# Kernel optimization log

Measured on AMD Instinct MI355X. Metric: run time of the kernel, lower is better.

The kernel has to match this reference:

```python
import math
import jax, jax.numpy as jnp
import numpy as np

N_HEAD = 16

def setup_inputs() -> dict:
    key = jax.random.key(0)
    ks = jax.random.split(key, 6)
    B, T, C = 8, 2048, 1024
    x = jax.random.normal(ks[0], (B, T, C), dtype=jnp.float32)
    # Linear weights stored as (in, out); scaled ~ standard init
    W_attn = jax.random.normal(ks[1], (C, 3 * C), dtype=jnp.float32) * (1.0 / math.sqrt(C))
    b_attn = jnp.zeros((3 * C,), dtype=jnp.float32)
    W_proj = jax.random.normal(ks[2], (C, C), dtype=jnp.float32) * (1.0 / math.sqrt(C))
    b_proj = jnp.zeros((C,), dtype=jnp.float32)
    # E/F: torch.randn in the original; scale by 0.02 so softmax is non-degenerate
    E = jax.random.normal(ks[3], (N_HEAD, 128, T), dtype=jnp.float32) * 0.02
    F = jax.random.normal(ks[4], (N_HEAD, 128, T), dtype=jnp.float32) * 0.02
    return {"x": x, "W_attn": W_attn, "b_attn": b_attn,
            "W_proj": W_proj, "b_proj": b_proj, "E": E, "F": F}

def reference(x, W_attn, b_attn, W_proj, b_proj, E, F):
    B, T, C = x.shape
    H = N_HEAD
    D = C // H
    scale = 1.0 / math.sqrt(D)
    qkv = x @ W_attn + b_attn                       # [B,T,3C]
    q, k, v = jnp.split(qkv, 3, axis=-1)
    # [B,T,C] -> [B,H,T,D]
    q = q.reshape(B, T, H, D).transpose(0, 2, 1, 3)
    k = k.reshape(B, T, H, D).transpose(0, 2, 1, 3)
    v = v.reshape(B, T, H, D).transpose(0, 2, 1, 3)
    Et = E[:, :, :T]                                # [H,k,T]
    Ft = F[:, :, :T]
    k_proj = jnp.einsum('hkt,bhtd->bhkd', Et, k)    # [B,H,k,D]
    v_proj = jnp.einsum('hkt,bhtd->bhkd', Ft, v)
    att = jnp.einsum('bhtd,bhkd->bhtk', q, k_proj) * scale
    att = jax.nn.softmax(att, axis=-1)              # dropout p=0 -> identity
    y = jnp.einsum('bhtk,bhkd->bhtd', att, v_proj)
    y = y.transpose(0, 2, 1, 3).reshape(B, T, C)
    return y @ W_proj + b_proj
```

## Files before the change

kernel.cpp:

```cpp
#include <hip/hip_runtime.h>
#include <math.h>


constexpr int B_ = 8, T_ = 2048, C_ = 1024, H_ = 16, D_ = 64, KP = 128;
constexpr int M_ = B_ * T_;
constexpr int C3 = 3 * C_;
constexpr int K_ = C_;
constexpr int TCH = 4;

typedef __attribute__((ext_vector_type(8))) short bf16x8;
typedef __attribute__((ext_vector_type(4))) float f32x4;

__device__ __forceinline__ unsigned short f2bf(float f) {
  unsigned u = __builtin_bit_cast(unsigned, f);
  u += 0x7FFFu + ((u >> 16) & 1u);
  return (unsigned short)(u >> 16);
}
__device__ __forceinline__ float bf2f(unsigned short h) {
  unsigned u = ((unsigned)h) << 16;
  return __builtin_bit_cast(float, u);
}

#define GLOAD_LDS16(gptr, lptr)                                                \
  __builtin_amdgcn_global_load_lds(                                            \
      (const __attribute__((address_space(1))) void*)(gptr),                   \
      (__attribute__((address_space(3))) void*)(lptr), 16, 0, 0)

__global__ __launch_bounds__(256) void cast_bf16(
    const float* __restrict__ in, unsigned short* __restrict__ hi, int n4)
{
  int i = blockIdx.x * 256 + threadIdx.x;
  if (i >= n4) return;
  const float4 v = reinterpret_cast<const float4*>(in)[i];
  ushort4 h;
  h.x = f2bf(v.x); h.y = f2bf(v.y); h.z = f2bf(v.z); h.w = f2bf(v.w);
  reinterpret_cast<ushort4*>(hi)[i] = h;
}

__global__ __launch_bounds__(256) void cast_tr(
    const float* __restrict__ W, unsigned short* __restrict__ Tb,
    int rows, int cols)
{
  __shared__ float tile[32][33];
  const int c0 = blockIdx.x * 32, r0 = blockIdx.y * 32;
  const int tx = threadIdx.x & 31, ty = threadIdx.x >> 5;
  #pragma unroll
  for (int i = 0; i < 4; ++i)
    tile[ty + i * 8][tx] = W[(size_t)(r0 + ty + i * 8) * cols + c0 + tx];
  __syncthreads();
  #pragma unroll
  for (int i = 0; i < 4; ++i) {
    const int cr = ty + i * 8;
    Tb[(size_t)(c0 + cr) * rows + r0 + tx] = f2bf(tile[tx][cr]);
  }
}

template <bool BFOUT>
__global__ __launch_bounds__(256) void gemm_mfma1(
    const unsigned short* __restrict__ A, const unsigned short* __restrict__ BT,
    const float* __restrict__ bias, float* __restrict__ Cf,
    unsigned short* __restrict__ Cb, int ldc)
{
  __shared__ unsigned short lds[2 * 4096];
  unsigned short* sA = lds;
  unsigned short* sB = lds + 4096;

  const int tid  = threadIdx.x;
  const int lane = tid & 63;
  const int wid  = tid >> 6;
  const int m0 = blockIdx.y * 128;
  const int n0 = blockIdx.x * 128;

  const int srow  = lane >> 2;
  const int skseg = (lane & 3) << 3;
  const int col  = lane & 15;
  const int quad = lane >> 4;
  const int Rm = (wid >> 1) << 6;
  const int Rn = (wid & 1) << 6;

  f32x4 acc[4][4];
  #pragma unroll
  for (int i = 0; i < 4; ++i)
    #pragma unroll
    for (int j = 0; j < 4; ++j)
      acc[i][j] = (f32x4){0.f, 0.f, 0.f, 0.f};

  for (int k0 = 0; k0 < K_; k0 += 32) {
    #pragma unroll
    for (int r = 0; r < 2; ++r) {
      const int chunk = (r << 2) + wid;
      const int row = (chunk << 4) + srow;
      const int ldso = chunk << 9;
      GLOAD_LDS16(A + (size_t)(m0 + row) * K_ + k0 + skseg, sA + ldso);
      GLOAD_LDS16(BT + (size_t)(n0 + row) * K_ + k0 + skseg, sB + ldso);
    }
    __syncthreads();

    bf16x8 a[4], b[4];
    #pragma unroll
    for (int t = 0; t < 4; ++t) {
      a[t] = *reinterpret_cast<const bf16x8*>(
          sA + ((Rm + (t << 4) + col) << 5) + (quad << 3));
      b[t] = *reinterpret_cast<const bf16x8*>(
          sB + ((Rn + (t << 4) + col) << 5) + (quad << 3));
    }
    #pragma unroll
    for (int i = 0; i < 4; ++i)
      #pragma unroll
      for (int j = 0; j < 4; ++j)
        acc[i][j] = __builtin_amdgcn_mfma_f32_16x16x32_bf16(a[i], b[j], acc[i][j], 0, 0, 0);
    __syncthreads();
  }

  #pragma unroll
  for (int i = 0; i < 4; ++i) {
    const int rbase = m0 + Rm + (i << 4) + (quad << 2);
    #pragma unroll
    for (int j = 0; j < 4; ++j) {
      const int c = n0 + Rn + (j << 4) + col;
      const float bv = bias[c];
      #pragma unroll
      for (int rg = 0; rg < 4; ++rg) {
        const float v = acc[i][j][rg] + bv;
        const size_t o = (size_t)(rbase + rg) * ldc + c;
        if constexpr (BFOUT) Cb[o] = f2bf(v);
        else Cf[o] = v;
      }
    }
  }
}

__global__ __launch_bounds__(256) void proj_mfma(
    const unsigned short* __restrict__ Eh, const unsigned short* __restrict__ kb,
    int ldk, float* __restrict__ part)
{
  __shared__ unsigned short sE[KP * 72];
  __shared__ unsigned short sK[D_ * 72];

  const int bh = blockIdx.x;
  const int tc = blockIdx.y;
  const int b = bh >> 4, h = bh & 15;
  const int tid = threadIdx.x;
  const int lane = tid & 63;
  const int w = tid >> 6;
  const int col = lane & 15;
  const int quad = lane >> 4;
  const int tq = tid >> 4;
  const int dq = tid & 15;

  f32x4 acc[2][4];
  #pragma unroll
  for (int i = 0; i < 2; ++i)
    #pragma unroll
    for (int j = 0; j < 4; ++j) acc[i][j] = (f32x4){0.f, 0.f, 0.f, 0.f};

  for (int s = 0; s < 8; ++s) {
    const int t0 = tc * 512 + s * 64;
    #pragma unroll
    for (int l = 0; l < 4; ++l) {
      const int idx = l * 256 + tid;
      const int kk = idx >> 3, seg = idx & 7;
      *reinterpret_cast<uint4*>(sE + kk * 72 + seg * 8) =
          *reinterpret_cast<const uint4*>(
              Eh + (size_t)(h * KP + kk) * T_ + t0 + seg * 8);
    }
    {
      const size_t gbase = (size_t)(b * T_ + t0 + tq * 4) * ldk + h * D_ + dq * 4;
      ushort4 r[4];
      #pragma unroll
      for (int rr = 0; rr < 4; ++rr)
        r[rr] = *reinterpret_cast<const ushort4*>(kb + gbase + (size_t)rr * ldk);
      #pragma unroll
      for (int c = 0; c < 4; ++c) {
        ushort4 t;
        t.x = (&r[0].x)[c]; t.y = (&r[1].x)[c];
        t.z = (&r[2].x)[c]; t.w = (&r[3].x)[c];
        *reinterpret_cast<ushort4*>(sK + (dq * 4 + c) * 72 + tq * 4) = t;
      }
    }
    __syncthreads();

    bf16x8 av[2][2];
    #pragma unroll
    for (int i = 0; i < 2; ++i)
      #pragma unroll
      for (int ks = 0; ks < 2; ++ks)
        av[i][ks] = *reinterpret_cast<const bf16x8*>(
            sE + ((w * 2 + i) * 16 + col) * 72 + ks * 32 + quad * 8);
    #pragma unroll
    for (int j = 0; j < 4; ++j)
      #pragma unroll
      for (int ks = 0; ks < 2; ++ks) {
        const bf16x8 bv = *reinterpret_cast<const bf16x8*>(
            sK + (j * 16 + col) * 72 + ks * 32 + quad * 8);
        #pragma unroll
        for (int i = 0; i < 2; ++i)
          acc[i][j] = __builtin_amdgcn_mfma_f32_16x16x32_bf16(av[i][ks], bv, acc[i][j], 0, 0, 0);
      }
    __syncthreads();
  }

  float* op = part + ((size_t)bh * TCH + tc) * (KP * D_);
  #pragma unroll
  for (int i = 0; i < 2; ++i) {
    const int kkb = w * 32 + i * 16 + quad * 4;
    #pragma unroll
    for (int j = 0; j < 4; ++j) {
      const int d = j * 16 + col;
      #pragma unroll
      for (int rg = 0; rg < 4; ++rg)
        op[(kkb + rg) * D_ + d] = acc[i][j][rg];
    }
  }
}

__global__ __launch_bounds__(256) void reduce_k(
    const float* __restrict__ part, unsigned short* __restrict__ kprojh)
{
  const int idx = blockIdx.x * 256 + threadIdx.x;
  const int bh = idx >> 13;
  const int i = idx & 8191;
  float s = 0.f;
  #pragma unroll
  for (int c = 0; c < TCH; ++c)
    s += part[((size_t)bh * TCH + c) * 8192 + i];
  kprojh[idx] = f2bf(s);
}

__global__ __launch_bounds__(256) void reduce_v(
    const float* __restrict__ part, unsigned short* __restrict__ vpTh)
{
  __shared__ float sums[KP * 66];
  const int bh = blockIdx.x;
  const int tid = threadIdx.x;
  #pragma unroll
  for (int j = 0; j < 32; ++j) {
    const int i = j * 256 + tid;
    float s = 0.f;
    #pragma unroll
    for (int c = 0; c < TCH; ++c)
      s += part[((size_t)bh * TCH + c) * 8192 + i];
    sums[(i >> 6) * 66 + (i & 63)] = s;
  }
  __syncthreads();
  #pragma unroll
  for (int j = 0; j < 32; ++j) {
    const int i = j * 256 + tid;
    vpTh[(size_t)bh * 8192 + i] = f2bf(sums[(i & 127) * 66 + (i >> 7)]);
  }
}

__global__ __launch_bounds__(256) void attn_mfma(
    const unsigned short* __restrict__ qkv, const unsigned short* __restrict__ kprojh,
    const unsigned short* __restrict__ vpTh, unsigned short* __restrict__ yh)
{
  __shared__ __attribute__((aligned(16))) char lds[35072];
  unsigned short* Qh = (unsigned short*)(lds);
  unsigned short* Kp = (unsigned short*)(lds + 9216);
  unsigned short* Vh = (unsigned short*)(lds);
  unsigned short* Ps = (unsigned short*)(lds + 17408);
  float* atts = (float*)(lds + 34816);

  const int tid  = threadIdx.x;
  const int lane = tid & 63;
  const int w    = tid >> 6;
  const int col  = lane & 15;
  const int quad = lane >> 4;
  const int bh = blockIdx.x >> 5;
  const int tch = blockIdx.x & 31;
  const int b = bh >> 4, h = bh & 15;
  const int t0 = tch * 64;

  {
    const unsigned short* qg = qkv + (size_t)(b * T_ + t0) * C3 + h * D_;
    #pragma unroll
    for (int l = 0; l < 4; ++l) {
      const int idx = l * 256 + tid;
      const int t = idx >> 4, dc = (idx & 15) << 2;
      *reinterpret_cast<ushort4*>(Qh + t * 72 + dc) =
          *reinterpret_cast<const ushort4*>(qg + (size_t)t * C3 + dc);
    }
    const unsigned short* kg = kprojh + (size_t)bh * 8192;
    #pragma unroll
    for (int l = 0; l < 8; ++l) {
      const int idx = l * 256 + tid;
      const int kk = idx >> 4, dc = (idx & 15) << 2;
      *reinterpret_cast<ushort4*>(Kp + kk * 72 + dc) =
          *reinterpret_cast<const ushort4*>(kg + kk * 64 + dc);
    }
  }
  __syncthreads();

  f32x4 s[8];
  #pragma unroll
  for (int i = 0; i < 8; ++i) s[i] = (f32x4){0.f, 0.f, 0.f, 0.f};
  bf16x8 bq[2];
  #pragma unroll
  for (int ks = 0; ks < 2; ++ks)
    bq[ks] = *reinterpret_cast<const bf16x8*>(
        Qh + (w * 16 + col) * 72 + ks * 32 + quad * 8);
  #pragma unroll
  for (int i = 0; i < 8; ++i)
    #pragma unroll
    for (int ks = 0; ks < 2; ++ks) {
      const bf16x8 a = *reinterpret_cast<const bf16x8*>(
          Kp + (i * 16 + col) * 72 + ks * 32 + quad * 8);
      s[i] = __builtin_amdgcn_mfma_f32_16x16x32_bf16(a, bq[ks], s[i], 0, 0, 0);
    }

  float mx = -3.0e38f;
  #pragma unroll
  for (int i = 0; i < 8; ++i)
    #pragma unroll
    for (int rg = 0; rg < 4; ++rg) {
      s[i][rg] *= 0.125f;
      mx = fmaxf(mx, s[i][rg]);
    }
  mx = fmaxf(mx, __shfl_xor(mx, 16));
  mx = fmaxf(mx, __shfl_xor(mx, 32));
  float sum = 0.f;
  #pragma unroll
  for (int i = 0; i < 8; ++i)
    #pragma unroll
    for (int rg = 0; rg < 4; ++rg) {
      const float e = __expf(s[i][rg] - mx);
      s[i][rg] = e;
      sum += e;
    }
  sum += __shfl_xor(sum, 16);
  sum += __shfl_xor(sum, 32);
  const float inv = 1.f / sum;
  __syncthreads();

  {
    const unsigned short* vg = vpTh + (size_t)bh * 8192;
    #pragma unroll
    for (int l = 0; l < 8; ++l) {
      const int idx = l * 256 + tid;
      const int d = idx >> 5, kc = (idx & 31) << 2;
      *reinterpret_cast<ushort4*>(Vh + d * 136 + kc) =
          *reinterpret_cast<const ushort4*>(vg + d * 128 + kc);
    }
  }
  #pragma unroll
  for (int i = 0; i < 8; ++i) {
    ushort4 hp;
    hp.x = f2bf(s[i][0]); hp.y = f2bf(s[i][1]);
    hp.z = f2bf(s[i][2]); hp.w = f2bf(s[i][3]);
    *reinterpret_cast<ushort4*>(Ps + (w * 16 + col) * 136 + i * 16 + quad * 4) = hp;
  }
  if (quad == 0) atts[w * 16 + col] = inv;
  __syncthreads();

  f32x4 y[4];
  #pragma unroll
  for (int j = 0; j < 4; ++j) y[j] = (f32x4){0.f, 0.f, 0.f, 0.f};
  bf16x8 ap[4];
  #pragma unroll
  for (int ks = 0; ks < 4; ++ks)
    ap[ks] = *reinterpret_cast<const bf16x8*>(
        Ps + (w * 16 + col) * 136 + ks * 32 + quad * 8);
  #pragma unroll
  for (int j = 0; j < 4; ++j)
    #pragma unroll
    for (int ks = 0; ks < 4; ++ks) {
      const bf16x8 bv = *reinterpret_cast<const bf16x8*>(
          Vh + (j * 16 + col) * 136 + ks * 32 + quad * 8);
      y[j] = __builtin_amdgcn_mfma_f32_16x16x32_bf16(ap[ks], bv, y[j], 0, 0, 0);
    }

  const f32x4 inv4 = *reinterpret_cast<const f32x4*>(atts + w * 16 + quad * 4);
  #pragma unroll
  for (int j = 0; j < 4; ++j)
    #pragma unroll
    for (int rg = 0; rg < 4; ++rg) {
      const int t = t0 + w * 16 + quad * 4 + rg;
      const int d = j * 16 + col;
      yh[(size_t)(b * T_ + t) * C_ + h * D_ + d] = f2bf(y[j][rg] * inv4[rg]);
    }
}

extern "C" void kernel_launch(void* const* d_in, const int* in_sizes, int n_in,
                              void* d_out, int out_size, void* d_ws, size_t ws_size,
                              hipStream_t stream) {
  (void)in_sizes; (void)n_in; (void)out_size; (void)ws_size;
  const float* x      = (const float*)d_in[0];
  const float* W_attn = (const float*)d_in[1];
  const float* b_attn = (const float*)d_in[2];
  const float* W_proj = (const float*)d_in[3];
  const float* b_proj = (const float*)d_in[4];
  const float* E      = (const float*)d_in[5];
  const float* F      = (const float*)d_in[6];
  float* out = (float*)d_out;

  unsigned short* xh   = (unsigned short*)d_ws;
  unsigned short* qkvh = xh + (size_t)M_ * C_;
  unsigned short* WaT  = qkvh + (size_t)M_ * C3;
  unsigned short* WpT  = WaT + (size_t)C3 * C_;
  unsigned short* Eh   = WpT + (size_t)C_ * C_;
  unsigned short* Fh   = Eh + (size_t)H_ * KP * T_;
  float* part = (float*)(Fh + (size_t)H_ * KP * T_);
  unsigned short* kprojh = (unsigned short*)(part + (size_t)B_ * H_ * TCH * KP * D_);
  unsigned short* vpTh   = kprojh + (size_t)B_ * H_ * KP * D_;
  unsigned short* yh = xh;

  cast_bf16<<<(M_ * C_ / 4 + 255) / 256, 256, 0, stream>>>(x, xh, M_ * C_ / 4);
  cast_bf16<<<(H_ * KP * T_ / 4 + 255) / 256, 256, 0, stream>>>(E, Eh, H_ * KP * T_ / 4);
  cast_bf16<<<(H_ * KP * T_ / 4 + 255) / 256, 256, 0, stream>>>(F, Fh, H_ * KP * T_ / 4);
  cast_tr<<<dim3(C3 / 32, C_ / 32), 256, 0, stream>>>(W_attn, WaT, C_, C3);
  cast_tr<<<dim3(C_ / 32, C_ / 32), 256, 0, stream>>>(W_proj, WpT, C_, C_);

  gemm_mfma1<true><<<dim3(C3 / 128, M_ / 128), 256, 0, stream>>>(
      xh, WaT, b_attn, nullptr, qkvh, C3);

  proj_mfma<<<dim3(B_ * H_, TCH), 256, 0, stream>>>(Eh, qkvh + C_, C3, part);
  reduce_k<<<(B_ * H_ * KP * D_) / 256, 256, 0, stream>>>(part, kprojh);

  proj_mfma<<<dim3(B_ * H_, TCH), 256, 0, stream>>>(Fh, qkvh + 2 * C_, C3, part);
  reduce_v<<<B_ * H_, 256, 0, stream>>>(part, vpTh);

  attn_mfma<<<B_ * H_ * (T_ / 64), 256, 0, stream>>>(qkvh, kprojh, vpTh, yh);

  gemm_mfma1<false><<<dim3(C_ / 128, M_ / 128), 256, 0, stream>>>(
      yh, WpT, b_proj, out, nullptr, C_);
}
```

Baseline: 416.1 us.

## Replace GEMM with 256x256 tile, 8-wave, double-buffered swizzled LDS pipeline

Swaps the 128x128 single-stage MFMA GEMM for a 256x256 tile kernel that uses 512 threads, a 64-wide K step and two 64KB LDS buffers. Global-to-LDS loads for later K tiles are interleaved with MFMA quadrants under explicit waitcnt and barrier control, and MFMA sections run at raised priority. The LDS layout is XOR-swizzled to avoid bank conflicts, and block IDs are remapped for L2 locality. The aim is more data reuse per byte loaded and overlap of load latency with compute in both large GEMMs. In exchange it relies on 128KB of LDS per block and fragile hand-written wait counts that could race or stall.

```diff
diff --git a/kernel.cpp b/kernel.cpp
--- a/kernel.cpp
+++ b/kernel.cpp
@@ -6,6 +6,7 @@
 constexpr int M_ = B_ * T_;
 constexpr int C3 = 3 * C_;
 constexpr int K_ = C_;
+constexpr int NT = K_ / 64;
 constexpr int TCH = 4;
 
 typedef __attribute__((ext_vector_type(8))) short bf16x8;
@@ -56,73 +57,172 @@
 }
 
 template <bool BFOUT>
-__global__ __launch_bounds__(256) void gemm_mfma1(
+__global__ __launch_bounds__(512, 2) void gemm256(
     const unsigned short* __restrict__ A, const unsigned short* __restrict__ BT,
     const float* __restrict__ bias, float* __restrict__ Cf,
     unsigned short* __restrict__ Cb, int ldc)
 {
-  __shared__ unsigned short lds[2 * 4096];
-  unsigned short* sA = lds;
-  unsigned short* sB = lds + 4096;
+  __shared__ __attribute__((aligned(16))) char lds[131072];
 
   const int tid  = threadIdx.x;
   const int lane = tid & 63;
-  const int wid  = tid >> 6;
-  const int m0 = blockIdx.y * 128;
-  const int n0 = blockIdx.x * 128;
-
-  const int srow  = lane >> 2;
-  const int skseg = (lane & 3) << 3;
+  const int w    = tid >> 6;
+  const int wr   = w >> 2;
+  const int wc   = w & 3;
   const int col  = lane & 15;
   const int quad = lane >> 4;
-  const int Rm = (wid >> 1) << 6;
-  const int Rn = (wid & 1) << 6;
-
-  f32x4 acc[4][4];
-  #pragma unroll
-  for (int i = 0; i < 4; ++i)
-    #pragma unroll
-    for (int j = 0; j < 4; ++j)
-      acc[i][j] = (f32x4){0.f, 0.f, 0.f, 0.f};
-
-  for (int k0 = 0; k0 < K_; k0 += 32) {
-    #pragma unroll
-    for (int r = 0; r < 2; ++r) {
-      const int chunk = (r << 2) + wid;
-      const int row = (chunk << 4) + srow;
-      const int ldso = chunk << 9;
-      GLOAD_LDS16(A + (size_t)(m0 + row) * K_ + k0 + skseg, sA + ldso);
-      GLOAD_LDS16(BT + (size_t)(n0 + row) * K_ + k0 + skseg, sB + ldso);
-    }
-    __syncthreads();
-
-    bf16x8 a[4], b[4];
-    #pragma unroll
-    for (int t = 0; t < 4; ++t) {
-      a[t] = *reinterpret_cast<const bf16x8*>(
-          sA + ((Rm + (t << 4) + col) << 5) + (quad << 3));
-      b[t] = *reinterpret_cast<const bf16x8*>(
-          sB + ((Rn + (t << 4) + col) << 5) + (quad << 3));
-    }
-    #pragma unroll
-    for (int i = 0; i < 4; ++i)
-      #pragma unroll
-      for (int j = 0; j < 4; ++j)
-        acc[i][j] = __builtin_amdgcn_mfma_f32_16x16x32_bf16(a[i], b[j], acc[i][j], 0, 0, 0);
-    __syncthreads();
-  }
-
-  #pragma unroll
-  for (int i = 0; i < 4; ++i) {
-    const int rbase = m0 + Rm + (i << 4) + (quad << 2);
-    #pragma unroll
-    for (int j = 0; j < 4; ++j) {
-      const int c = n0 + Rn + (j << 4) + col;
-      const float bv = bias[c];
+
+  const int ntx = ldc >> 8;
+  int wg = blockIdx.x;
+  wg = (wg & 7) * (gridDim.x >> 3) + (wg >> 3);
+  const int bx = wg % ntx, by = wg / ntx;
+  const int m0 = by << 8, n0 = bx << 8;
+
+  int mOff[2], nOff[2], csh[2];
+  #pragma unroll
+  for (int l = 0; l < 2; ++l) {
+    const int rl = w * 16 + l * 8 + (lane >> 3);
+    mOff[l] = (rl >> 6) * 128 + (rl & 63);
+    nOff[l] = (rl >> 5) * 64 + (rl & 31);
+    csh[l]  = ((lane & 7) * 8) ^ (((lane >> 5) & 1) << 4) ^ (l << 3);
+  }
+
+#define STAGE_A(H, KT0, BUFSEL)                                                \
+  { const int kb_ = (KT0) * 64;                                                \
+    _Pragma("unroll")                                                          \
+    for (int l = 0; l < 2; ++l)                                                \
+      GLOAD_LDS16(A + (size_t)(m0 + mOff[l] + (H) * 64) * K_ + kb_ + csh[l],   \
+                  lds + (BUFSEL) * 65536 + (H) * 16384 + w * 2048 + l * 1024); }
+
+#define STAGE_B(H, KT0, BUFSEL)                                                \
+  { const int kb_ = (KT0) * 64;                                                \
+    _Pragma("unroll")                                                          \
+    for (int l = 0; l < 2; ++l)                                                \
+      GLOAD_LDS16(BT + (size_t)(n0 + nOff[l] + (H) * 32) * K_ + kb_ + csh[l],  \
+                  lds + (BUFSEL) * 65536 + 32768 + (H) * 16384 + w * 2048 +    \
+                      l * 1024); }
+
+  const int qsw = (quad * 16) ^ ((col & 4) << 3) ^ ((col & 8) << 1);
+  const int aB0 = (wr * 64 + col) * 128;
+  const int aB1 = (128 + wr * 64 + col) * 128;
+  const int bB0 = 32768 + (wc * 32 + col) * 128;
+  const int bB1 = 32768 + (128 + wc * 32 + col) * 128;
+
+  f32x4 acc[8][4];
+  #pragma unroll
+  for (int a = 0; a < 8; ++a)
+    #pragma unroll
+    for (int c = 0; c < 4; ++c)
+      acc[a][c] = (f32x4){0.f, 0.f, 0.f, 0.f};
+
+  bf16x8 av[4][2], b0v[2][2], b1v[2][2];
+
+#define MFMA_Q(QM, QN, BV)                                                     \
+  __builtin_amdgcn_s_setprio(1);                                               \
+  _Pragma("unroll")                                                            \
+  for (int j = 0; j < 2; ++j)                                                  \
+    _Pragma("unroll")                                                          \
+    for (int ks = 0; ks < 2; ++ks)                                             \
+      _Pragma("unroll")                                                        \
+      for (int i = 0; i < 4; ++i)                                              \
+        acc[(QM) * 4 + i][(QN) * 2 + j] =                                      \
+            __builtin_amdgcn_mfma_f32_16x16x32_bf16(                           \
+                av[i][ks], BV[j][ks], acc[(QM) * 4 + i][(QN) * 2 + j], 0, 0, 0);\
+  __builtin_amdgcn_s_setprio(0);
+
+  STAGE_A(0, 0, 0);
+  STAGE_B(0, 0, 0);
+  STAGE_B(1, 0, 0);
+  STAGE_A(1, 0, 0);
+  asm volatile("s_waitcnt vmcnt(4)" ::: "memory");
+  STAGE_A(0, 1, 1);
+  STAGE_B(0, 1, 1);
+  STAGE_B(1, 1, 1);
+  asm volatile("s_waitcnt vmcnt(6)" ::: "memory");
+  __builtin_amdgcn_s_barrier();
+
+#define TILE(KT, CUR)                                                          \
+  {                                                                            \
+    const char* cb = lds + (CUR) * 65536;                                      \
+                       \
+    _Pragma("unroll")                                                          \
+    for (int i = 0; i < 4; ++i)                                                \
+      _Pragma("unroll")                                                        \
+      for (int ks = 0; ks < 2; ++ks)                                           \
+        av[i][ks] = *reinterpret_cast<const bf16x8*>(                          \
+            cb + aB0 + i * 2048 + ks * 64 + qsw);                              \
+    _Pragma("unroll")                                                          \
+    for (int j = 0; j < 2; ++j)                                                \
+      _Pragma("unroll")                                                        \
+      for (int ks = 0; ks < 2; ++ks)                                           \
+        b0v[j][ks] = *reinterpret_cast<const bf16x8*>(                         \
+            cb + bB0 + j * 2048 + ks * 64 + qsw);                              \
+    if ((KT) + 1 < NT) { STAGE_A(1, (KT) + 1, (CUR) ^ 1); }                    \
+    asm volatile("s_waitcnt lgkmcnt(8)" ::: "memory");                         \
+    __builtin_amdgcn_s_barrier();                                              \
+    asm volatile("s_waitcnt lgkmcnt(0)" ::: "memory");                         \
+    __builtin_amdgcn_sched_barrier(0);                                         \
+    MFMA_Q(0, 0, b0v);                                                         \
+    __builtin_amdgcn_s_barrier();                                              \
+                        \
+    _Pragma("unroll")                                                          \
+    for (int j = 0; j < 2; ++j)                                                \
+      _Pragma("unroll")                                                        \
+      for (int ks = 0; ks < 2; ++ks)                                           \
+        b1v[j][ks] = *reinterpret_cast<const bf16x8*>(                         \
+            cb + bB1 + j * 2048 + ks * 64 + qsw);                              \
+    if ((KT) + 2 < NT) { STAGE_A(0, (KT) + 2, (CUR)); }                        \
+    __builtin_amdgcn_s_barrier();                                              \
+    asm volatile("s_waitcnt lgkmcnt(0)" ::: "memory");                         \
+    __builtin_amdgcn_sched_barrier(0);                                         \
+    MFMA_Q(0, 1, b1v);                                                         \
+    __builtin_amdgcn_s_barrier();                                              \
+                        \
+    _Pragma("unroll")                                                          \
+    for (int i = 0; i < 4; ++i)                                                \
+      _Pragma("unroll")                                                        \
+      for (int ks = 0; ks < 2; ++ks)                                           \
+        av[i][ks] = *reinterpret_cast<const bf16x8*>(                          \
+            cb + aB1 + i * 2048 + ks * 64 + qsw);                              \
+    if ((KT) + 2 < NT) { STAGE_B(0, (KT) + 2, (CUR)); }                        \
+    __builtin_amdgcn_s_barrier();                                              \
+    asm volatile("s_waitcnt lgkmcnt(0)" ::: "memory");                         \
+    __builtin_amdgcn_sched_barrier(0);                                         \
+    MFMA_Q(1, 1, b1v);                                                         \
+    __builtin_amdgcn_s_barrier();                                              \
+        \
+    if ((KT) + 2 < NT) { STAGE_B(1, (KT) + 2, (CUR)); }                        \
+    __builtin_amdgcn_s_barrier();                                              \
+    __builtin_amdgcn_sched_barrier(0);                                         \
+    MFMA_Q(1, 0, b0v);                                                         \
+    if ((KT) < NT - 2) {                                                       \
+      asm volatile("s_waitcnt vmcnt(6)" ::: "memory");                         \
+    } else if ((KT) == NT - 2) {                                               \
+      asm volatile("s_waitcnt vmcnt(0)" ::: "memory");                         \
+    }                                                                          \
+    __builtin_amdgcn_s_barrier();                                              \
+  }
+
+  for (int kt = 0; kt < NT; kt += 2) {
+    TILE(kt, 0);
+    TILE(kt + 1, 1);
+  }
+#undef TILE
+#undef MFMA_Q
+#undef STAGE_A
+#undef STAGE_B
+
+  #pragma unroll
+  for (int a = 0; a < 8; ++a) {
+    const int r = m0 + wr * 128 + (a >> 2) * 64 + (a & 3) * 16 + quad * 4;
+    #pragma unroll
+    for (int c = 0; c < 4; ++c) {
+      const int cc = n0 + wc * 64 + (c >> 1) * 32 + (c & 1) * 16 + col;
+      const float bv = bias[cc];
       #pragma unroll
       for (int rg = 0; rg < 4; ++rg) {
-        const float v = acc[i][j][rg] + bv;
-        const size_t o = (size_t)(rbase + rg) * ldc + c;
+        const float v = acc[a][c][rg] + bv;
+        const size_t o = (size_t)(r + rg) * ldc + cc;
         if constexpr (BFOUT) Cb[o] = f2bf(v);
         else Cf[o] = v;
       }
@@ -410,7 +510,7 @@
   cast_tr<<<dim3(C3 / 32, C_ / 32), 256, 0, stream>>>(W_attn, WaT, C_, C3);
   cast_tr<<<dim3(C_ / 32, C_ / 32), 256, 0, stream>>>(W_proj, WpT, C_, C_);
 
-  gemm_mfma1<true><<<dim3(C3 / 128, M_ / 128), 256, 0, stream>>>(
+  gemm256<true><<<dim3((M_ / 256) * (C3 / 256)), 512, 0, stream>>>(
       xh, WaT, b_attn, nullptr, qkvh, C3);
 
   proj_mfma<<<dim3(B_ * H_, TCH), 256, 0, stream>>>(Eh, qkvh + C_, C3, part);
@@ -421,6 +521,6 @@
 
   attn_mfma<<<B_ * H_ * (T_ / 64), 256, 0, stream>>>(qkvh, kprojh, vpTh, yh);
 
-  gemm_mfma1<false><<<dim3(C_ / 128, M_ / 128), 256, 0, stream>>>(
+  gemm256<false><<<dim3((M_ / 256) * (C_ / 256)), 512, 0, stream>>>(
       yh, WpT, b_proj, out, nullptr, C_);
 }
```

After: 402.3 us. 3.3% less time.

## Rewrite GEMMs as 128x256 double-buffered pipelined kernels with XCD-aware tile swizzle

Applied to the files above, without the earlier changes.

Replaces the single-buffered 128x128 MFMA GEMM with a 512-thread 128x256 tile kernel. It double-buffers LDS, staggers global-to-LDS loads between two MFMA phases under explicit waitcnt and barriers, and raises wave priority during MFMA. Block indices are remapped across the 8 XCDs for better L2 locality. This is meant to hide global load latency and improve data reuse in both the QKV and output projections, at the cost of complex manual synchronisation and larger LDS and register use.

```diff
diff --git a/kernel.cpp b/kernel.cpp
--- a/kernel.cpp
+++ b/kernel.cpp
@@ -6,6 +6,7 @@
 constexpr int M_ = B_ * T_;
 constexpr int C3 = 3 * C_;
 constexpr int K_ = C_;
+constexpr int NT = K_ / 32;
 constexpr int TCH = 4;
 
 typedef __attribute__((ext_vector_type(8))) short bf16x8;
@@ -56,27 +57,44 @@
 }
 
 template <bool BFOUT>
-__global__ __launch_bounds__(256) void gemm_mfma1(
+__global__ __launch_bounds__(512, 4) void gemm128(
     const unsigned short* __restrict__ A, const unsigned short* __restrict__ BT,
     const float* __restrict__ bias, float* __restrict__ Cf,
     unsigned short* __restrict__ Cb, int ldc)
 {
-  __shared__ unsigned short lds[2 * 4096];
-  unsigned short* sA = lds;
-  unsigned short* sB = lds + 4096;
+  __shared__ __attribute__((aligned(16))) char lds[49152];
 
   const int tid  = threadIdx.x;
   const int lane = tid & 63;
-  const int wid  = tid >> 6;
-  const int m0 = blockIdx.y * 128;
-  const int n0 = blockIdx.x * 128;
-
-  const int srow  = lane >> 2;
-  const int skseg = (lane & 3) << 3;
+  const int w    = tid >> 6;
+  const int wr   = w >> 2;
+  const int wc   = w & 3;
   const int col  = lane & 15;
   const int quad = lane >> 4;
-  const int Rm = (wid >> 1) << 6;
-  const int Rn = (wid & 1) << 6;
+
+  const int ntx = ldc >> 8;
+  int wg = blockIdx.x;
+  wg = (wg & 7) * (gridDim.x >> 3) + (wg >> 3);
+  const int bx = wg % ntx, by = wg / ntx;
+  const int m0 = by << 7, n0 = bx << 8;
+
+  const int kq   = quad * 8;
+  const int fnB0 = (w >> 1) * 4 + (w & 1);
+  const int fnB1 = fnB0 + 2;
+  const unsigned short* Asrc  = A  + (size_t)(m0 + w * 16 + col) * K_ + kq;
+  const unsigned short* B0src = BT + (size_t)(n0 + fnB0 * 16 + col) * K_ + kq;
+  const unsigned short* B1src = BT + (size_t)(n0 + fnB1 * 16 + col) * K_ + kq;
+  const int dA  = w * 1024 + lane * 16;
+  const int dB0 = 8192 + fnB0 * 1024 + lane * 16;
+  const int dB1 = 8192 + fnB1 * 1024 + lane * 16;
+
+#define STG_A(KT, BUF)  GLOAD_LDS16(Asrc  + (KT) * 32, lds + (BUF) * 24576 + dA)
+#define STG_B0(KT, BUF) GLOAD_LDS16(B0src + (KT) * 32, lds + (BUF) * 24576 + dB0)
+#define STG_B1(KT, BUF) GLOAD_LDS16(B1src + (KT) * 32, lds + (BUF) * 24576 + dB1)
+
+  const int laneB = lane * 16;
+  const int aOff = wr * 4096 + laneB;
+  const int bOff = 8192 + wc * 4096 + laneB;
 
   f32x4 acc[4][4];
   #pragma unroll
@@ -85,44 +103,74 @@
     for (int j = 0; j < 4; ++j)
       acc[i][j] = (f32x4){0.f, 0.f, 0.f, 0.f};
 
-  for (int k0 = 0; k0 < K_; k0 += 32) {
-    #pragma unroll
-    for (int r = 0; r < 2; ++r) {
-      const int chunk = (r << 2) + wid;
-      const int row = (chunk << 4) + srow;
-      const int ldso = chunk << 9;
-      GLOAD_LDS16(A + (size_t)(m0 + row) * K_ + k0 + skseg, sA + ldso);
-      GLOAD_LDS16(BT + (size_t)(n0 + row) * K_ + k0 + skseg, sB + ldso);
-    }
-    __syncthreads();
-
-    bf16x8 a[4], b[4];
-    #pragma unroll
-    for (int t = 0; t < 4; ++t) {
-      a[t] = *reinterpret_cast<const bf16x8*>(
-          sA + ((Rm + (t << 4) + col) << 5) + (quad << 3));
-      b[t] = *reinterpret_cast<const bf16x8*>(
-          sB + ((Rn + (t << 4) + col) << 5) + (quad << 3));
-    }
-    #pragma unroll
-    for (int i = 0; i < 4; ++i)
-      #pragma unroll
-      for (int j = 0; j < 4; ++j)
-        acc[i][j] = __builtin_amdgcn_mfma_f32_16x16x32_bf16(a[i], b[j], acc[i][j], 0, 0, 0);
-    __syncthreads();
-  }
+  bf16x8 av[4], bv[4];
+
+  STG_A(0, 0); STG_B0(0, 0); STG_B1(0, 0);
+  STG_A(1, 1); STG_B0(1, 1);
+  asm volatile("s_waitcnt vmcnt(2)" ::: "memory");
+  __builtin_amdgcn_s_barrier();
+
+#define TILE(KT, CUR)                                                          \
+  {                                                                            \
+    const char* cb = lds + (CUR) * 24576;                                      \
+                        \
+    _Pragma("unroll")                                                          \
+    for (int i = 0; i < 4; ++i)                                                \
+      av[i] = *reinterpret_cast<const bf16x8*>(cb + aOff + i * 1024);          \
+    bv[0] = *reinterpret_cast<const bf16x8*>(cb + bOff);                       \
+    bv[1] = *reinterpret_cast<const bf16x8*>(cb + bOff + 1024);                \
+    if ((KT) + 1 < NT) { STG_B1((KT) + 1, (CUR) ^ 1); }                        \
+    __builtin_amdgcn_s_barrier();                                              \
+    __builtin_amdgcn_s_setprio(1);                                             \
+    _Pragma("unroll")                                                          \
+    for (int j = 0; j < 2; ++j)                                                \
+      _Pragma("unroll")                                                        \
+      for (int i = 0; i < 4; ++i)                                              \
+        acc[i][j] = __builtin_amdgcn_mfma_f32_16x16x32_bf16(                   \
+            av[i], bv[j], acc[i][j], 0, 0, 0);                                 \
+    __builtin_amdgcn_s_setprio(0);                                             \
+    __builtin_amdgcn_s_barrier();                                              \
+           \
+    bv[2] = *reinterpret_cast<const bf16x8*>(cb + bOff + 2048);                \
+    bv[3] = *reinterpret_cast<const bf16x8*>(cb + bOff + 3072);                \
+    if ((KT) + 2 < NT) { STG_A((KT) + 2, (CUR)); STG_B0((KT) + 2, (CUR)); }    \
+    __builtin_amdgcn_s_barrier();                                              \
+    __builtin_amdgcn_s_setprio(1);                                             \
+    _Pragma("unroll")                                                          \
+    for (int j = 2; j < 4; ++j)                                                \
+      _Pragma("unroll")                                                        \
+      for (int i = 0; i < 4; ++i)                                              \
+        acc[i][j] = __builtin_amdgcn_mfma_f32_16x16x32_bf16(                   \
+            av[i], bv[j], acc[i][j], 0, 0, 0);                                 \
+    __builtin_amdgcn_s_setprio(0);                                             \
+    if ((KT) < NT - 2) {                                                       \
+      asm volatile("s_waitcnt vmcnt(2)" ::: "memory");                         \
+    } else if ((KT) == NT - 2) {                                               \
+      asm volatile("s_waitcnt vmcnt(0)" ::: "memory");                         \
+    }                                                                          \
+    __builtin_amdgcn_s_barrier();                                              \
+  }
+
+  for (int kt = 0; kt < NT; kt += 2) {
+    TILE(kt, 0);
+    TILE(kt + 1, 1);
+  }
+#undef TILE
+#undef STG_A
+#undef STG_B0
+#undef STG_B1
 
   #pragma unroll
   for (int i = 0; i < 4; ++i) {
-    const int rbase = m0 + Rm + (i << 4) + (quad << 2);
+    const int r = m0 + wr * 64 + i * 16 + quad * 4;
     #pragma unroll
     for (int j = 0; j < 4; ++j) {
-      const int c = n0 + Rn + (j << 4) + col;
-      const float bv = bias[c];
+      const int cc = n0 + wc * 64 + j * 16 + col;
+      const float bvb = bias[cc];
       #pragma unroll
       for (int rg = 0; rg < 4; ++rg) {
-        const float v = acc[i][j][rg] + bv;
-        const size_t o = (size_t)(rbase + rg) * ldc + c;
+        const float v = acc[i][j][rg] + bvb;
+        const size_t o = (size_t)(r + rg) * ldc + cc;
         if constexpr (BFOUT) Cb[o] = f2bf(v);
         else Cf[o] = v;
       }
@@ -410,7 +458,7 @@
   cast_tr<<<dim3(C3 / 32, C_ / 32), 256, 0, stream>>>(W_attn, WaT, C_, C3);
   cast_tr<<<dim3(C_ / 32, C_ / 32), 256, 0, stream>>>(W_proj, WpT, C_, C_);
 
-  gemm_mfma1<true><<<dim3(C3 / 128, M_ / 128), 256, 0, stream>>>(
+  gemm128<true><<<dim3((M_ / 128) * (C3 / 256)), 512, 0, stream>>>(
       xh, WaT, b_attn, nullptr, qkvh, C3);
 
   proj_mfma<<<dim3(B_ * H_, TCH), 256, 0, stream>>>(Eh, qkvh + C_, C3, part);
@@ -421,6 +469,6 @@
 
   attn_mfma<<<B_ * H_ * (T_ / 64), 256, 0, stream>>>(qkvh, kprojh, vpTh, yh);
 
-  gemm_mfma1<false><<<dim3(C_ / 128, M_ / 128), 256, 0, stream>>>(
+  gemm128<false><<<dim3((M_ / 128) * (C_ / 256)), 512, 0, stream>>>(
       yh, WpT, b_proj, out, nullptr, C_);
 }
```

Result: slower. 424.8 us (+2.1%).
